# Optimization experiments

Measured on AMD Instinct MI355X. Metric: run time of the kernel, lower is better.

Reference implementation:

```python
import jax, jax.numpy as jnp
import numpy as np

BSZ, L, H, P = 8, 4096, 512, 256  # batch, seq len, features, complex state dim (conj_sym)
DT_MIN, DT_MAX = 1e-3, 1e-1


def setup_inputs() -> dict:
    key = jax.random.key(0)
    k_u, k_B, k_C, k_D, k_dt = jax.random.split(key, 5)
    u = jax.random.normal(k_u, (BSZ, L, H), dtype=jnp.float32)
    # HiPPO-like stable init for the diagonal state matrix
    Lambda_re = -0.5 * jnp.ones((P,), dtype=jnp.float32)
    Lambda_im = jnp.pi * jnp.arange(P, dtype=jnp.float32)
    # lecun-normal-ish scaling for real/imag parts of B (fan_in = H) and C (fan_in = P)
    B = jax.random.normal(k_B, (P, H, 2), dtype=jnp.float32) / jnp.sqrt(2.0 * H)
    C = jax.random.normal(k_C, (H, P, 2), dtype=jnp.float32) / jnp.sqrt(2.0 * P)
    D = jax.random.normal(k_D, (H,), dtype=jnp.float32)
    log_step = jax.random.uniform(k_dt, (P, 1), dtype=jnp.float32,
                                  minval=jnp.log(DT_MIN), maxval=jnp.log(DT_MAX))
    return {"u": u, "Lambda_re": Lambda_re, "Lambda_im": Lambda_im,
            "B": B, "C": C, "D": D, "log_step": log_step}


def _binop(q_i, q_j):
    """Associative binary operator for diagonal linear recurrence."""
    A_i, b_i = q_i
    A_j, b_j = q_j
    return (A_j * A_i, A_j * b_i + b_j)


def reference(u, Lambda_re, Lambda_im, B, C, D, log_step):
    # --- setup / discretization (zero-order hold) ---
    Lambda = (Lambda_re + 1j * Lambda_im).astype(jnp.complex64)      # (P,)
    B_tilde = (B[..., 0] + 1j * B[..., 1]).astype(jnp.complex64)     # (P,H)
    C_tilde = (C[..., 0] + 1j * C[..., 1]).astype(jnp.complex64)     # (H,P)
    step = jnp.exp(log_step[:, 0])                                   # (P,)
    Lambda_bar = jnp.exp(Lambda * step)                              # (P,)
    B_bar = ((Lambda_bar - 1.0) / Lambda)[:, None] * B_tilde         # (P,H)

    # --- parallel scan over the sequence (diagonal SSM) ---
    Bu = jnp.einsum('blh,ph->blp', u, B_bar)                         # (B,L,P) complex64
    Lam = jnp.broadcast_to(Lambda_bar, Bu.shape)                     # (B,L,P)
    _, xs = jax.lax.associative_scan(_binop, (Lam, Bu), axis=1)      # (B,L,P)

    # --- emissions (factor 2 from conjugate symmetry) + feedthrough ---
    ys = 2.0 * jnp.einsum('blp,hp->blh', xs, C_tilde).real + D * u   # (B,L,H)
    return jax.nn.gelu(ys)
```

## Files before the change

kernel.cpp:

```cpp
#include <hip/hip_runtime.h>
#include <cstdint>
#include <cstddef>

typedef unsigned short u16;
typedef short short8 __attribute__((ext_vector_type(8)));
typedef float floatx4 __attribute__((ext_vector_type(4)));

#define DEVINL __device__ __forceinline__

static constexpr int BSZ = 8, SEQL = 4096, H = 512, P = 256;
static constexpr int M = BSZ * SEQL;
static constexpr int KD = 512;
static constexpr int ND = 512;
static constexpr int CHUNK = 128;
static constexpr int NCH = SEQL / CHUNK;

DEVINL u16 f2bf(float f) {
  union { float f; unsigned u; } v; v.f = f;
  unsigned r = (v.u + 0x7fffu + ((v.u >> 16) & 1u)) >> 16;
  return (u16)r;
}
DEVINL float bf2f(u16 h) {
  union { unsigned u; float f; } v; v.u = ((unsigned)h) << 16; return v.f;
}

DEVINL void gload_lds16(const void* g, void* l) {
  __builtin_amdgcn_global_load_lds(
      (const __attribute__((address_space(1))) unsigned*)g,
      (__attribute__((address_space(3))) unsigned*)l, 16, 0, 0);
}

DEVINL float2 lam_of(int p, const float* __restrict__ Lre, const float* __restrict__ Lim,
                     const float* __restrict__ lstep) {
  float lr = Lre[p], li = Lim[p];
  float st = expf(lstep[p]);
  float mag = expf(lr * st);
  float ang = li * st;
  return make_float2(mag * cosf(ang), mag * sinf(ang));
}

__global__ void prep_kernel(const float2* __restrict__ Bin, const float* __restrict__ Cin,
                            const float* __restrict__ Lre, const float* __restrict__ Lim,
                            const float* __restrict__ lstep,
                            u16* __restrict__ bt1, u16* __restrict__ bt2) {
  int bid = blockIdx.x;
  if (bid < 512) {
    int idx = bid * 256 + threadIdx.x;
    int p = idx / H, h = idx % H;
    float lr = Lre[p], li = Lim[p];
    float st = expf(lstep[p]);
    float mag = expf(lr * st);
    float ang = li * st;
    float cr = mag * cosf(ang), ci = mag * sinf(ang);
    float a = cr - 1.0f, b = ci;
    float den = lr * lr + li * li;
    float fr = (a * lr + b * li) / den;
    float fi = (b * lr - a * li) / den;
    float2 bv = Bin[(size_t)p * H + h];
    float br = fr * bv.x - fi * bv.y;
    float bi = fr * bv.y + fi * bv.x;
    bt1[(size_t)(2 * p) * H + h]     = f2bf(br);
    bt1[(size_t)(2 * p + 1) * H + h] = f2bf(bi);
  } else {
    int idx = (bid - 512) * 256 + threadIdx.x;
    float c = Cin[idx];
    float v = (idx & 1) ? -2.0f * c : 2.0f * c;
    bt2[idx] = f2bf(v);
  }
}

__global__ __launch_bounds__(256, 3) void gemm0(const float* __restrict__ Af32,
                                                const u16* __restrict__ Bt,
                                                u16* __restrict__ outBf,
                                                const float* __restrict__ Lre,
                                                const float* __restrict__ Lim,
                                                const float* __restrict__ lstep,
                                                float2* __restrict__ carry) {
  __shared__ float Asf[2][128 * 32];
  __shared__ u16   Bs[2][128 * 32];
  const int tid = threadIdx.x;
  const int bm = blockIdx.x, bn = blockIdx.y;
  const int wave = tid >> 6, lane = tid & 63;
  const int quad = lane >> 4, l16 = lane & 15;
  const int wm = (wave & 1) << 6, wn = (wave >> 1) << 6;

  floatx4 acc[4][4] = {};

  const float* Ab = Af32 + (size_t)bm * 128 * KD;
  const u16*   Bb = Bt + (size_t)bn * 128 * KD;
  const int srowA = tid >> 3;
  const int scolA = (((tid & 7) ^ ((tid >> 3) & 7)) << 2);
  const int srowB = tid >> 2;
  const int scolB = (tid & 3) << 3;

#define STAGE0(buf, kofs)                                                                     \
  do {                                                                                        \
    gload_lds16(Ab + (size_t)srowA * KD + (kofs) + scolA,        &Asf[buf][tid * 4]);         \
    gload_lds16(Ab + (size_t)(srowA + 32) * KD + (kofs) + scolA, &Asf[buf][1024 + tid * 4]);  \
    gload_lds16(Ab + (size_t)(srowA + 64) * KD + (kofs) + scolA, &Asf[buf][2048 + tid * 4]);  \
    gload_lds16(Ab + (size_t)(srowA + 96) * KD + (kofs) + scolA, &Asf[buf][3072 + tid * 4]);  \
    gload_lds16(Bb + (size_t)srowB * KD + (kofs) + scolB,        &Bs[buf][tid * 8]);          \
    gload_lds16(Bb + (size_t)(srowB + 64) * KD + (kofs) + scolB, &Bs[buf][2048 + tid * 8]);   \
  } while (0)

  STAGE0(0, 0);
  asm volatile("s_waitcnt vmcnt(0)" ::: "memory");
  __builtin_amdgcn_sched_barrier(0);
  __builtin_amdgcn_s_barrier();

  const int c0 = ((quad << 1) ^ (l16 & 7));
  const int c1 = c0 ^ 1;

  int cur = 0;
  for (int k0 = 0; k0 < KD; k0 += 32) {
    if (k0 + 32 < KD) STAGE0(cur ^ 1, k0 + 32);

    short8 af[4], bfr[4];
#pragma unroll
    for (int t = 0; t < 4; t++) {
      const float* rowp = &Asf[cur][(wm + t * 16 + l16) * 32];
      float4 a0 = *(const float4*)(rowp + c0 * 4);
      float4 a1 = *(const float4*)(rowp + c1 * 4);
      af[t][0] = (short)f2bf(a0.x); af[t][1] = (short)f2bf(a0.y);
      af[t][2] = (short)f2bf(a0.z); af[t][3] = (short)f2bf(a0.w);
      af[t][4] = (short)f2bf(a1.x); af[t][5] = (short)f2bf(a1.y);
      af[t][6] = (short)f2bf(a1.z); af[t][7] = (short)f2bf(a1.w);
    }
#pragma unroll
    for (int t = 0; t < 4; t++)
      bfr[t] = *(const short8*)&Bs[cur][(wn + t * 16 + l16) * 32 + quad * 8];

    asm volatile("s_waitcnt lgkmcnt(0)" ::: "memory");
    __builtin_amdgcn_sched_barrier(0);

    __builtin_amdgcn_s_setprio(1);
#pragma unroll
    for (int tm = 0; tm < 4; tm++)
#pragma unroll
      for (int tn = 0; tn < 4; tn++)
        acc[tm][tn] = __builtin_amdgcn_mfma_f32_16x16x32_bf16(af[tm], bfr[tn], acc[tm][tn], 0, 0, 0);
    __builtin_amdgcn_s_setprio(0);

    asm volatile("s_waitcnt vmcnt(0)" ::: "memory");
    __builtin_amdgcn_sched_barrier(0);
    __builtin_amdgcn_s_barrier();
    cur ^= 1;
  }
#undef STAGE0

  const int row_base = bm * 128 + wm + quad * 4;
  const int col_base = bn * 128 + wn + l16;
#pragma unroll
  for (int tm = 0; tm < 4; tm++)
#pragma unroll
    for (int tn = 0; tn < 4; tn++) {
      int n = col_base + tn * 16;
#pragma unroll
      for (int r = 0; r < 4; r++) {
        int m = row_base + tm * 16 + r;
        outBf[(size_t)m * ND + n] = f2bf(acc[tm][tn][r]);
      }
    }

  __syncthreads();
  if (tid < 64) {
    const int lp = tid;
    const int p = bn * 64 + lp;
    const int cix = bm & 31, b = bm >> 5;
    float2 lm = lam_of(p, Lre, Lim, lstep);
    const u16* tb = outBf + (size_t)(bm * 128) * ND + bn * 128 + 2 * lp;
    float xr = 0.f, xi = 0.f;
    for (int l0 = 0; l0 < 128; l0 += 8) {
      unsigned w[8];
#pragma unroll
      for (int t = 0; t < 8; t++)
        w[t] = *(const unsigned*)(tb + (size_t)(l0 + t) * ND);
#pragma unroll
      for (int t = 0; t < 8; t++) {
        float br = bf2f((u16)(w[t] & 0xffffu));
        float bi = bf2f((u16)(w[t] >> 16));
        float nr = lm.x * xr - lm.y * xi + br;
        float ni = lm.x * xi + lm.y * xr + bi;
        xr = nr; xi = ni;
      }
    }
    carry[((size_t)b * NCH + cix) * P + p] = make_float2(xr, xi);
  }
}

__global__ __launch_bounds__(256, 4) void gemm1(const u16* __restrict__ A,
                                                const u16* __restrict__ Bt,
                                                float* __restrict__ outF,
                                                const float* __restrict__ Dv,
                                                const float* __restrict__ U32) {
  __shared__ u16 As[2][128 * 32];
  __shared__ u16 Bs[2][128 * 32];
  const int tid = threadIdx.x;
  const int bm = blockIdx.x, bn = blockIdx.y;
  const int wave = tid >> 6, lane = tid & 63;
  const int quad = lane >> 4, l16 = lane & 15;
  const int wm = (wave & 1) << 6, wn = (wave >> 1) << 6;

  floatx4 acc[4][4] = {};

  const u16* Ab = A + (size_t)bm * 128 * KD;
  const u16* Bb = Bt + (size_t)bn * 128 * KD;
  const int srow = tid >> 2;
  const int scol = (tid & 3) << 3;

#define STAGE1(buf, kofs)                                                                  \
  do {                                                                                     \
    gload_lds16(Ab + (size_t)srow * KD + (kofs) + scol,        &As[buf][tid * 8]);         \
    gload_lds16(Ab + (size_t)(srow + 64) * KD + (kofs) + scol, &As[buf][2048 + tid * 8]);  \
    gload_lds16(Bb + (size_t)srow * KD + (kofs) + scol,        &Bs[buf][tid * 8]);         \
    gload_lds16(Bb + (size_t)(srow + 64) * KD + (kofs) + scol, &Bs[buf][2048 + tid * 8]);  \
  } while (0)

  STAGE1(0, 0);
  asm volatile("s_waitcnt vmcnt(0)" ::: "memory");
  __builtin_amdgcn_sched_barrier(0);
  __builtin_amdgcn_s_barrier();

  int cur = 0;
  for (int k0 = 0; k0 < KD; k0 += 32) {
    if (k0 + 32 < KD) STAGE1(cur ^ 1, k0 + 32);

    short8 af[4], bfr[4];
#pragma unroll
    for (int t = 0; t < 4; t++)
      af[t] = *(const short8*)&As[cur][(wm + t * 16 + l16) * 32 + quad * 8];
#pragma unroll
    for (int t = 0; t < 4; t++)
      bfr[t] = *(const short8*)&Bs[cur][(wn + t * 16 + l16) * 32 + quad * 8];

    asm volatile("s_waitcnt lgkmcnt(0)" ::: "memory");
    __builtin_amdgcn_sched_barrier(0);

    __builtin_amdgcn_s_setprio(1);
#pragma unroll
    for (int tm = 0; tm < 4; tm++)
#pragma unroll
      for (int tn = 0; tn < 4; tn++)
        acc[tm][tn] = __builtin_amdgcn_mfma_f32_16x16x32_bf16(af[tm], bfr[tn], acc[tm][tn], 0, 0, 0);
    __builtin_amdgcn_s_setprio(0);

    asm volatile("s_waitcnt vmcnt(0)" ::: "memory");
    __builtin_amdgcn_sched_barrier(0);
    __builtin_amdgcn_s_barrier();
    cur ^= 1;
  }
#undef STAGE1

  const int row_base = bm * 128 + wm + quad * 4;
  const int col_base = bn * 128 + wn + l16;
  float dv[4];
#pragma unroll
  for (int tn = 0; tn < 4; tn++) dv[tn] = Dv[col_base + tn * 16];
#pragma unroll
  for (int tm = 0; tm < 4; tm++)
#pragma unroll
    for (int tn = 0; tn < 4; tn++) {
      int n = col_base + tn * 16;
#pragma unroll
      for (int r = 0; r < 4; r++) {
        int m = row_base + tm * 16 + r;
        float ys = acc[tm][tn][r] + dv[tn] * U32[(size_t)m * ND + n];
        float zz = ys + 0.044715f * (ys * ys * ys);
        float e = __builtin_amdgcn_exp2f(-2.3022082f * zz);
        outF[(size_t)m * ND + n] = ys * __builtin_amdgcn_rcpf(1.0f + e);
      }
    }
}

__global__ __launch_bounds__(256) void scan_apply(u16* __restrict__ Bu,
                                                  const float* __restrict__ Lre,
                                                  const float* __restrict__ Lim,
                                                  const float* __restrict__ lstep,
                                                  const float2* __restrict__ carry) {
  int p = threadIdx.x;
  int c = blockIdx.x;
  int b = blockIdx.y;
  float2 lm = lam_of(p, Lre, Lim, lstep);
  float ar = lm.x, ai = lm.y;
#pragma unroll
  for (int i = 0; i < 7; i++) { float nr = ar * ar - ai * ai, ni = 2.f * ar * ai; ar = nr; ai = ni; }
  float pr = 0.f, pi = 0.f;
  const float2* cb_base = carry + (size_t)b * NCH * P + p;
  for (int j0 = 0; j0 < c; j0 += 16) {
    float2 cb[16];
#pragma unroll
    for (int t = 0; t < 16; t++) {
      int j = j0 + t;
      int jc = j < c ? j : c - 1;
      cb[t] = cb_base[(size_t)jc * P];
    }
#pragma unroll
    for (int t = 0; t < 16; t++) {
      bool real = (j0 + t) < c;
      float mr = real ? ar : 1.0f;
      float mi = real ? ai : 0.0f;
      float cx = real ? cb[t].x : 0.0f;
      float cy = real ? cb[t].y : 0.0f;
      float nr = mr * pr - mi * pi + cx;
      float ni = mr * pi + mi * pr + cy;
      pr = nr; pi = ni;
    }
  }
  float xr = pr, xi = pi;
  u16* base = Bu + ((size_t)b * SEQL + (size_t)c * CHUNK) * 512 + 2 * p;
  for (int l0 = 0; l0 < CHUNK; l0 += 8) {
    unsigned w[8];
#pragma unroll
    for (int t = 0; t < 8; t++)
      w[t] = *(const unsigned*)(base + (size_t)(l0 + t) * 512);
#pragma unroll
    for (int t = 0; t < 8; t++) {
      float br = bf2f((u16)(w[t] & 0xffffu));
      float bi = bf2f((u16)(w[t] >> 16));
      float nr = lm.x * xr - lm.y * xi + br;
      float ni = lm.x * xi + lm.y * xr + bi;
      xr = nr; xi = ni;
      *(unsigned*)(base + (size_t)(l0 + t) * 512) = (unsigned)f2bf(nr) | ((unsigned)f2bf(ni) << 16);
    }
  }
}

extern "C" void kernel_launch(void* const* d_in, const int* in_sizes, int n_in,
                              void* d_out, int out_size, void* d_ws, size_t ws_size,
                              hipStream_t stream) {
  const float* u      = (const float*)d_in[0];
  const float* Lre    = (const float*)d_in[1];
  const float* Lim    = (const float*)d_in[2];
  const float* Bin    = (const float*)d_in[3];
  const float* Cin    = (const float*)d_in[4];
  const float* Dv     = (const float*)d_in[5];
  const float* lstep  = (const float*)d_in[6];
  float* out          = (float*)d_out;

  char* ws = (char*)d_ws;
  u16*    bt1    = (u16*)   (ws + 0);
  u16*    bt2    = (u16*)   (ws + 524288);
  u16*    Bu     = (u16*)   (ws + 1048576);
  float2* carry  = (float2*)(ws + 34603008);

  prep_kernel<<<1536, 256, 0, stream>>>((const float2*)Bin, Cin, Lre, Lim, lstep, bt1, bt2);

  gemm0<<<dim3(M / 128, ND / 128), 256, 0, stream>>>(u, bt1, Bu, Lre, Lim, lstep, carry);

  scan_apply<<<dim3(NCH, BSZ), 256, 0, stream>>>(Bu, Lre, Lim, lstep, carry);

  gemm1<<<dim3(M / 128, ND / 128), 256, 0, stream>>>(Bu, bt2, out, Dv, u);
}
```

Measured before the change: 221.3 us.

## Pre-convert u to bf16, compute chunk carries from registers, halve chunk size

Adds a kernel that converts u to bf16 once, so gemm0 stages bf16 A directly and gemm1 reads bf16 u for the feedthrough term. The per-chunk carry is now computed from the MFMA accumulators in registers using precomputed powers of lambda, combined with cross-lane shuffles. This replaces the serial 64-thread rescan of the stored tile. The chunk size drops to 64, and lambda tables are computed once in prep_kernel. The cost is an extra pass over u plus a workspace copy of it, and the feedthrough term now uses a bf16-rounded u.

```diff
diff --git a/kernel.cpp b/kernel.cpp
--- a/kernel.cpp
+++ b/kernel.cpp
@@ -12,7 +12,7 @@
 static constexpr int M = BSZ * SEQL;
 static constexpr int KD = 512;
 static constexpr int ND = 512;
-static constexpr int CHUNK = 128;
+static constexpr int CHUNK = 64;
 static constexpr int NCH = SEQL / CHUNK;
 
 DEVINL u16 f2bf(float f) {
@@ -23,6 +23,9 @@
 DEVINL float bf2f(u16 h) {
   union { unsigned u; float f; } v; v.u = ((unsigned)h) << 16; return v.f;
 }
+DEVINL float2 cmul(float2 a, float2 b) {
+  return make_float2(a.x * b.x - a.y * b.y, a.x * b.y + a.y * b.x);
+}
 
 DEVINL void gload_lds16(const void* g, void* l) {
   __builtin_amdgcn_global_load_lds(
@@ -30,19 +33,12 @@
       (__attribute__((address_space(3))) unsigned*)l, 16, 0, 0);
 }
 
-DEVINL float2 lam_of(int p, const float* __restrict__ Lre, const float* __restrict__ Lim,
-                     const float* __restrict__ lstep) {
-  float lr = Lre[p], li = Lim[p];
-  float st = expf(lstep[p]);
-  float mag = expf(lr * st);
-  float ang = li * st;
-  return make_float2(mag * cosf(ang), mag * sinf(ang));
-}
-
 __global__ void prep_kernel(const float2* __restrict__ Bin, const float* __restrict__ Cin,
                             const float* __restrict__ Lre, const float* __restrict__ Lim,
                             const float* __restrict__ lstep,
-                            u16* __restrict__ bt1, u16* __restrict__ bt2) {
+                            u16* __restrict__ bt1, u16* __restrict__ bt2,
+                            float2* __restrict__ lamt, float2* __restrict__ lam4t,
+                            float2* __restrict__ lam13t) {
   int bid = blockIdx.x;
   if (bid < 512) {
     int idx = bid * 256 + threadIdx.x;
@@ -61,138 +57,41 @@
     float bi = fr * bv.y + fi * bv.x;
     bt1[(size_t)(2 * p) * H + h]     = f2bf(br);
     bt1[(size_t)(2 * p + 1) * H + h] = f2bf(bi);
-  } else {
+  } else if (bid < 1536) {
     int idx = (bid - 512) * 256 + threadIdx.x;
     float c = Cin[idx];
     float v = (idx & 1) ? -2.0f * c : 2.0f * c;
     bt2[idx] = f2bf(v);
-  }
-}
-
-__global__ __launch_bounds__(256, 3) void gemm0(const float* __restrict__ Af32,
+  } else {
+    int p = threadIdx.x;
+    float lr = Lre[p], li = Lim[p];
+    float st = expf(lstep[p]);
+    float mag = expf(lr * st);
+    float ang = li * st;
+    float2 lm = make_float2(mag * cosf(ang), mag * sinf(ang));
+    float2 l2 = cmul(lm, lm);
+    float2 l4 = cmul(l2, l2);
+    float2 l8 = cmul(l4, l4);
+    float2 l13 = cmul(cmul(l8, l4), lm);
+    lamt[p] = lm; lam4t[p] = l4; lam13t[p] = l13;
+  }
+}
+
+__global__ void ucvt_kernel(const float4* __restrict__ uin, ushort4* __restrict__ ubf) {
+  int idx = blockIdx.x * 256 + threadIdx.x;
+  float4 f = uin[idx];
+  ushort4 o;
+  o.x = f2bf(f.x); o.y = f2bf(f.y); o.z = f2bf(f.z); o.w = f2bf(f.w);
+  ubf[idx] = o;
+}
+
+__global__ __launch_bounds__(256, 4) void gemm0(const u16* __restrict__ A,
                                                 const u16* __restrict__ Bt,
                                                 u16* __restrict__ outBf,
-                                                const float* __restrict__ Lre,
-                                                const float* __restrict__ Lim,
-                                                const float* __restrict__ lstep,
+                                                const float2* __restrict__ lamt,
+                                                const float2* __restrict__ lam4t,
+                                                const float2* __restrict__ lam13t,
                                                 float2* __restrict__ carry) {
-  __shared__ float Asf[2][128 * 32];
-  __shared__ u16   Bs[2][128 * 32];
-  const int tid = threadIdx.x;
-  const int bm = blockIdx.x, bn = blockIdx.y;
-  const int wave = tid >> 6, lane = tid & 63;
-  const int quad = lane >> 4, l16 = lane & 15;
-  const int wm = (wave & 1) << 6, wn = (wave >> 1) << 6;
-
-  floatx4 acc[4][4] = {};
-
-  const float* Ab = Af32 + (size_t)bm * 128 * KD;
-  const u16*   Bb = Bt + (size_t)bn * 128 * KD;
-  const int srowA = tid >> 3;
-  const int scolA = (((tid & 7) ^ ((tid >> 3) & 7)) << 2);
-  const int srowB = tid >> 2;
-  const int scolB = (tid & 3) << 3;
-
-#define STAGE0(buf, kofs)                                                                     \
-  do {                                                                                        \
-    gload_lds16(Ab + (size_t)srowA * KD + (kofs) + scolA,        &Asf[buf][tid * 4]);         \
-    gload_lds16(Ab + (size_t)(srowA + 32) * KD + (kofs) + scolA, &Asf[buf][1024 + tid * 4]);  \
-    gload_lds16(Ab + (size_t)(srowA + 64) * KD + (kofs) + scolA, &Asf[buf][2048 + tid * 4]);  \
-    gload_lds16(Ab + (size_t)(srowA + 96) * KD + (kofs) + scolA, &Asf[buf][3072 + tid * 4]);  \
-    gload_lds16(Bb + (size_t)srowB * KD + (kofs) + scolB,        &Bs[buf][tid * 8]);          \
-    gload_lds16(Bb + (size_t)(srowB + 64) * KD + (kofs) + scolB, &Bs[buf][2048 + tid * 8]);   \
-  } while (0)
-
-  STAGE0(0, 0);
-  asm volatile("s_waitcnt vmcnt(0)" ::: "memory");
-  __builtin_amdgcn_sched_barrier(0);
-  __builtin_amdgcn_s_barrier();
-
-  const int c0 = ((quad << 1) ^ (l16 & 7));
-  const int c1 = c0 ^ 1;
-
-  int cur = 0;
-  for (int k0 = 0; k0 < KD; k0 += 32) {
-    if (k0 + 32 < KD) STAGE0(cur ^ 1, k0 + 32);
-
-    short8 af[4], bfr[4];
-#pragma unroll
-    for (int t = 0; t < 4; t++) {
-      const float* rowp = &Asf[cur][(wm + t * 16 + l16) * 32];
-      float4 a0 = *(const float4*)(rowp + c0 * 4);
-      float4 a1 = *(const float4*)(rowp + c1 * 4);
-      af[t][0] = (short)f2bf(a0.x); af[t][1] = (short)f2bf(a0.y);
-      af[t][2] = (short)f2bf(a0.z); af[t][3] = (short)f2bf(a0.w);
-      af[t][4] = (short)f2bf(a1.x); af[t][5] = (short)f2bf(a1.y);
-      af[t][6] = (short)f2bf(a1.z); af[t][7] = (short)f2bf(a1.w);
-    }
-#pragma unroll
-    for (int t = 0; t < 4; t++)
-      bfr[t] = *(const short8*)&Bs[cur][(wn + t * 16 + l16) * 32 + quad * 8];
-
-    asm volatile("s_waitcnt lgkmcnt(0)" ::: "memory");
-    __builtin_amdgcn_sched_barrier(0);
-
-    __builtin_amdgcn_s_setprio(1);
-#pragma unroll
-    for (int tm = 0; tm < 4; tm++)
-#pragma unroll
-      for (int tn = 0; tn < 4; tn++)
-        acc[tm][tn] = __builtin_amdgcn_mfma_f32_16x16x32_bf16(af[tm], bfr[tn], acc[tm][tn], 0, 0, 0);
-    __builtin_amdgcn_s_setprio(0);
-
-    asm volatile("s_waitcnt vmcnt(0)" ::: "memory");
-    __builtin_amdgcn_sched_barrier(0);
-    __builtin_amdgcn_s_barrier();
-    cur ^= 1;
-  }
-#undef STAGE0
-
-  const int row_base = bm * 128 + wm + quad * 4;
-  const int col_base = bn * 128 + wn + l16;
-#pragma unroll
-  for (int tm = 0; tm < 4; tm++)
-#pragma unroll
-    for (int tn = 0; tn < 4; tn++) {
-      int n = col_base + tn * 16;
-#pragma unroll
-      for (int r = 0; r < 4; r++) {
-        int m = row_base + tm * 16 + r;
-        outBf[(size_t)m * ND + n] = f2bf(acc[tm][tn][r]);
-      }
-    }
-
-  __syncthreads();
-  if (tid < 64) {
-    const int lp = tid;
-    const int p = bn * 64 + lp;
-    const int cix = bm & 31, b = bm >> 5;
-    float2 lm = lam_of(p, Lre, Lim, lstep);
-    const u16* tb = outBf + (size_t)(bm * 128) * ND + bn * 128 + 2 * lp;
-    float xr = 0.f, xi = 0.f;
-    for (int l0 = 0; l0 < 128; l0 += 8) {
-      unsigned w[8];
-#pragma unroll
-      for (int t = 0; t < 8; t++)
-        w[t] = *(const unsigned*)(tb + (size_t)(l0 + t) * ND);
-#pragma unroll
-      for (int t = 0; t < 8; t++) {
-        float br = bf2f((u16)(w[t] & 0xffffu));
-        float bi = bf2f((u16)(w[t] >> 16));
-        float nr = lm.x * xr - lm.y * xi + br;
-        float ni = lm.x * xi + lm.y * xr + bi;
-        xr = nr; xi = ni;
-      }
-    }
-    carry[((size_t)b * NCH + cix) * P + p] = make_float2(xr, xi);
-  }
-}
-
-__global__ __launch_bounds__(256, 4) void gemm1(const u16* __restrict__ A,
-                                                const u16* __restrict__ Bt,
-                                                float* __restrict__ outF,
-                                                const float* __restrict__ Dv,
-                                                const float* __restrict__ U32) {
   __shared__ u16 As[2][128 * 32];
   __shared__ u16 Bs[2][128 * 32];
   const int tid = threadIdx.x;
@@ -208,6 +107,116 @@
   const int srow = tid >> 2;
   const int scol = (tid & 3) << 3;
 
+#define STAGE0(buf, kofs)                                                                  \
+  do {                                                                                     \
+    gload_lds16(Ab + (size_t)srow * KD + (kofs) + scol,        &As[buf][tid * 8]);         \
+    gload_lds16(Ab + (size_t)(srow + 64) * KD + (kofs) + scol, &As[buf][2048 + tid * 8]);  \
+    gload_lds16(Bb + (size_t)srow * KD + (kofs) + scol,        &Bs[buf][tid * 8]);         \
+    gload_lds16(Bb + (size_t)(srow + 64) * KD + (kofs) + scol, &Bs[buf][2048 + tid * 8]);  \
+  } while (0)
+
+  STAGE0(0, 0);
+  asm volatile("s_waitcnt vmcnt(0)" ::: "memory");
+  __builtin_amdgcn_sched_barrier(0);
+  __builtin_amdgcn_s_barrier();
+
+  int cur = 0;
+  for (int k0 = 0; k0 < KD; k0 += 32) {
+    if (k0 + 32 < KD) STAGE0(cur ^ 1, k0 + 32);
+
+    short8 af[4], bfr[4];
+#pragma unroll
+    for (int t = 0; t < 4; t++)
+      af[t] = *(const short8*)&As[cur][(wm + t * 16 + l16) * 32 + quad * 8];
+#pragma unroll
+    for (int t = 0; t < 4; t++)
+      bfr[t] = *(const short8*)&Bs[cur][(wn + t * 16 + l16) * 32 + quad * 8];
+
+    asm volatile("s_waitcnt lgkmcnt(0)" ::: "memory");
+    __builtin_amdgcn_sched_barrier(0);
+
+    __builtin_amdgcn_s_setprio(1);
+#pragma unroll
+    for (int tm = 0; tm < 4; tm++)
+#pragma unroll
+      for (int tn = 0; tn < 4; tn++)
+        acc[tm][tn] = __builtin_amdgcn_mfma_f32_16x16x32_bf16(af[tm], bfr[tn], acc[tm][tn], 0, 0, 0);
+    __builtin_amdgcn_s_setprio(0);
+
+    asm volatile("s_waitcnt vmcnt(0)" ::: "memory");
+    __builtin_amdgcn_sched_barrier(0);
+    __builtin_amdgcn_s_barrier();
+    cur ^= 1;
+  }
+#undef STAGE0
+
+  const int row_base = bm * 128 + wm + quad * 4;
+  const int col_base = bn * 128 + wn + l16;
+#pragma unroll
+  for (int tm = 0; tm < 4; tm++)
+#pragma unroll
+    for (int tn = 0; tn < 4; tn++) {
+      int n = col_base + tn * 16;
+#pragma unroll
+      for (int r = 0; r < 4; r++) {
+        int m = row_base + tm * 16 + r;
+        outBf[(size_t)m * ND + n] = f2bf(acc[tm][tn][r]);
+      }
+    }
+
+  {
+    const int half = wave & 1;
+    const int cix = ((bm & 31) << 1) | half;
+    const int b = bm >> 5;
+#pragma unroll
+    for (int tn = 0; tn < 4; tn++) {
+      const int n = col_base + tn * 16;
+      const int p = n >> 1;
+      const float2 lm = lamt[p];
+      const float2 l4 = lam4t[p];
+      const float2 l13 = lam13t[p];
+      float2 s = make_float2(0.f, 0.f);
+#pragma unroll
+      for (int tm = 0; tm < 4; tm++)
+#pragma unroll
+        for (int r = 0; r < 4; r++) {
+          float2 mult = (r == 0) ? l13 : lm;
+          s = cmul(s, mult);
+          s.x += acc[tm][tn][r];
+        }
+#pragma unroll
+      for (int i = 0; i < 3; i++)
+        if (i < 3 - quad) s = cmul(s, l4);
+      s.x += __shfl_xor(s.x, 16); s.y += __shfl_xor(s.y, 16);
+      s.x += __shfl_xor(s.x, 32); s.y += __shfl_xor(s.y, 32);
+      float oR = __shfl_xor(s.x, 1), oI = __shfl_xor(s.y, 1);
+      if (!(lane & 1)) {
+        carry[((size_t)b * NCH + cix) * P + p] = make_float2(s.x - oI, s.y + oR);
+      }
+    }
+  }
+}
+
+__global__ __launch_bounds__(256, 4) void gemm1(const u16* __restrict__ A,
+                                                const u16* __restrict__ Bt,
+                                                float* __restrict__ outF,
+                                                const float* __restrict__ Dv,
+                                                const u16* __restrict__ ubf) {
+  __shared__ u16 As[2][128 * 32];
+  __shared__ u16 Bs[2][128 * 32];
+  const int tid = threadIdx.x;
+  const int bm = blockIdx.x, bn = blockIdx.y;
+  const int wave = tid >> 6, lane = tid & 63;
+  const int quad = lane >> 4, l16 = lane & 15;
+  const int wm = (wave & 1) << 6, wn = (wave >> 1) << 6;
+
+  floatx4 acc[4][4] = {};
+
+  const u16* Ab = A + (size_t)bm * 128 * KD;
+  const u16* Bb = Bt + (size_t)bn * 128 * KD;
+  const int srow = tid >> 2;
+  const int scol = (tid & 3) << 3;
+
 #define STAGE1(buf, kofs)                                                                  \
   do {                                                                                     \
     gload_lds16(Ab + (size_t)srow * KD + (kofs) + scol,        &As[buf][tid * 8]);         \
@@ -264,7 +273,8 @@
 #pragma unroll
       for (int r = 0; r < 4; r++) {
         int m = row_base + tm * 16 + r;
-        float ys = acc[tm][tn][r] + dv[tn] * U32[(size_t)m * ND + n];
+        float uv = bf2f(ubf[(size_t)m * ND + n]);
+        float ys = acc[tm][tn][r] + dv[tn] * uv;
         float zz = ys + 0.044715f * (ys * ys * ys);
         float e = __builtin_amdgcn_exp2f(-2.3022082f * zz);
         outF[(size_t)m * ND + n] = ys * __builtin_amdgcn_rcpf(1.0f + e);
@@ -273,17 +283,15 @@
 }
 
 __global__ __launch_bounds__(256) void scan_apply(u16* __restrict__ Bu,
-                                                  const float* __restrict__ Lre,
-                                                  const float* __restrict__ Lim,
-                                                  const float* __restrict__ lstep,
+                                                  const float2* __restrict__ lamt,
                                                   const float2* __restrict__ carry) {
   int p = threadIdx.x;
   int c = blockIdx.x;
   int b = blockIdx.y;
-  float2 lm = lam_of(p, Lre, Lim, lstep);
+  float2 lm = lamt[p];
   float ar = lm.x, ai = lm.y;
 #pragma unroll
-  for (int i = 0; i < 7; i++) { float nr = ar * ar - ai * ai, ni = 2.f * ar * ai; ar = nr; ai = ni; }
+  for (int i = 0; i < 6; i++) { float nr = ar * ar - ai * ai, ni = 2.f * ar * ai; ar = nr; ai = ni; }
   float pr = 0.f, pi = 0.f;
   const float2* cb_base = carry + (size_t)b * NCH * P + p;
   for (int j0 = 0; j0 < c; j0 += 16) {
@@ -340,14 +348,20 @@
   char* ws = (char*)d_ws;
   u16*    bt1    = (u16*)   (ws + 0);
   u16*    bt2    = (u16*)   (ws + 524288);
-  u16*    Bu     = (u16*)   (ws + 1048576);
-  float2* carry  = (float2*)(ws + 34603008);
-
-  prep_kernel<<<1536, 256, 0, stream>>>((const float2*)Bin, Cin, Lre, Lim, lstep, bt1, bt2);
-
-  gemm0<<<dim3(M / 128, ND / 128), 256, 0, stream>>>(u, bt1, Bu, Lre, Lim, lstep, carry);
-
-  scan_apply<<<dim3(NCH, BSZ), 256, 0, stream>>>(Bu, Lre, Lim, lstep, carry);
-
-  gemm1<<<dim3(M / 128, ND / 128), 256, 0, stream>>>(Bu, bt2, out, Dv, u);
-}
+  float2* lamt   = (float2*)(ws + 1048576);
+  float2* lam4t  = (float2*)(ws + 1050624);
+  float2* lam13t = (float2*)(ws + 1052672);
+  u16*    ubf    = (u16*)   (ws + 1054720);
+  u16*    Bu     = (u16*)   (ws + 34609152);
+  float2* carry  = (float2*)(ws + 68163584);
+
+  prep_kernel<<<1537, 256, 0, stream>>>((const float2*)Bin, Cin, Lre, Lim, lstep,
+                                        bt1, bt2, lamt, lam4t, lam13t);
+  ucvt_kernel<<<(M * H / 4) / 256, 256, 0, stream>>>((const float4*)u, (ushort4*)ubf);
+
+  gemm0<<<dim3(M / 128, ND / 128), 256, 0, stream>>>(ubf, bt1, Bu, lamt, lam4t, lam13t, carry);
+
+  scan_apply<<<dim3(NCH, BSZ), 256, 0, stream>>>(Bu, lamt, carry);
+
+  gemm1<<<dim3(M / 128, ND / 128), 256, 0, stream>>>(Bu, bt2, out, Dv, ubf);
+}
```

New measurement: 236.3 us. +6.8%, slower.
